# Kernel tuning notes

Hardware: AMD Instinct MI355X
Metric: run time of the kernel (lower is better)

The kernel has to match this reference:

```python
import jax, jax.numpy as jnp
import numpy as np

DIM = 128
B, LQ, LK = 8, 2048, 2048


def setup_inputs() -> dict:
    key = jax.random.key(0)
    k1, k2, k3 = jax.random.split(key, 3)
    output = jax.random.normal(k1, (B, LQ, DIM), dtype=jnp.float32)
    context = jax.random.normal(k2, (B, LK, DIM), dtype=jnp.float32)
    mask = jax.random.randint(k3, (B, LQ, LK), 0, 2).astype(jnp.bool_)
    return {"output": output, "context": context, "mask": mask}


def reference(output, context, mask):
    temperature = jnp.asarray(np.power(DIM, 0.5), dtype=output.dtype)
    # scores: [B, Lq, Lk]
    attn = jnp.einsum('bqd,bkd->bqk', output, context) / temperature
    attn = jnp.where(mask, -jnp.inf, attn)
    out_attn = jax.nn.log_softmax(attn, axis=-1)
    p = jax.nn.softmax(attn, axis=-1)
    # dropout is identity in eval/reference mode
    out = jnp.einsum('bqk,bkd->bqd', p, context)
    return (out, out_attn)
```

## Files before the change

kernel.cpp:

```cpp
#include <hip/hip_runtime.h>
#include <cstdint>


#define DIMV 128
constexpr int BB = 8;
constexpr int LQ = 2048;
constexpr int LK = 2048;
constexpr float RTEMP = 0.08838834764831843f;

typedef _Float16 half8 __attribute__((ext_vector_type(8)));
typedef _Float16 half4v __attribute__((ext_vector_type(4)));
typedef float float4v __attribute__((ext_vector_type(4)));

__global__ void cvt_kernel(const float* __restrict__ q, const float* __restrict__ k,
                           _Float16* __restrict__ q16, _Float16* __restrict__ k16) {
    int idx = blockIdx.x * blockDim.x + threadIdx.x;
    constexpr int NV = BB * LQ * DIMV / 4;
    const float4* src;
    _Float16* dst;
    int v;
    if (idx < NV) { src = (const float4*)q; dst = q16; v = idx; }
    else          { src = (const float4*)k; dst = k16; v = idx - NV; }
    float4 f = src[v];
    half4v h;
    h[0] = (_Float16)f.x; h[1] = (_Float16)f.y; h[2] = (_Float16)f.z; h[3] = (_Float16)f.w;
    *(half4v*)(dst + (size_t)v * 4) = h;
}

__global__ void transp_kernel(const float* __restrict__ ctx, _Float16* __restrict__ vT) {
    __shared__ _Float16 tile[64][DIMV + 2];
    int b = blockIdx.x >> 5;
    int k0 = (blockIdx.x & 31) * 64;
    const float4* src = (const float4*)(ctx + ((size_t)b * LK + k0) * DIMV);
    for (int i = 0; i < 8; i++) {
        int off = threadIdx.x + i * 256;
        float4 f = src[off];
        int elem = off * 4;
        int row = elem >> 7, col = elem & 127;
        tile[row][col + 0] = (_Float16)f.x;
        tile[row][col + 1] = (_Float16)f.y;
        tile[row][col + 2] = (_Float16)f.z;
        tile[row][col + 3] = (_Float16)f.w;
    }
    __syncthreads();
    int d = threadIdx.x >> 1;
    int koff = (threadIdx.x & 1) * 32;
    _Float16* dst = vT + ((size_t)b * DIMV + d) * LK + k0 + koff;
    for (int c = 0; c < 4; c++) {
        half8 h;
        for (int j = 0; j < 8; j++) h[j] = tile[koff + c * 8 + j][d];
        *(half8*)(dst + c * 8) = h;
    }
}

__global__ __launch_bounds__(256, 1)
void attn_kernel(const unsigned char* __restrict__ mask,
                 const _Float16* __restrict__ q16, const _Float16* __restrict__ k16,
                 const _Float16* __restrict__ vT,
                 float* __restrict__ out, float* __restrict__ out_attn) {
    constexpr int TQ = 32;
    constexpr int SSTR = 2056;
    __shared__ __attribute__((aligned(16))) _Float16 S[TQ * SSTR];
    __shared__ float redm[4][TQ];
    __shared__ float mfin[TQ];

    const int tid  = threadIdx.x;
    const int wave = tid >> 6;
    const int lane = tid & 63;
    const int l16  = lane & 15;
    const int quad = lane >> 4;

    const int b  = blockIdx.x >> 6;
    const int q0 = (blockIdx.x & 63) * TQ;

    const _Float16* qbase = q16 + ((size_t)b * LQ + q0) * DIMV;
    const _Float16* kbase = k16 + (size_t)b * LK * DIMV;

    half8 afrag[2][4];
    for (int rt = 0; rt < 2; rt++)
        for (int kk = 0; kk < 4; kk++)
            afrag[rt][kk] = *(const half8*)(qbase + (size_t)(rt * 16 + l16) * DIMV + kk * 32 + quad * 8);

    float mloc[2][4];
    for (int rt = 0; rt < 2; rt++)
        for (int r = 0; r < 4; r++) mloc[rt][r] = -__builtin_inff();

    for (int ch = 0; ch < 8; ch++) {
        const int colbase = wave * 512 + ch * 64;
        float4v acc[4][2];
        for (int ct = 0; ct < 4; ct++)
            for (int rt = 0; rt < 2; rt++)
                acc[ct][rt] = (float4v){0.f, 0.f, 0.f, 0.f};
        for (int ct = 0; ct < 4; ct++) {
            for (int kk = 0; kk < 4; kk++) {
                half8 bf = *(const half8*)(kbase + (size_t)(colbase + ct * 16 + l16) * DIMV + kk * 32 + quad * 8);
                acc[ct][0] = __builtin_amdgcn_mfma_f32_16x16x32_f16(afrag[0][kk], bf, acc[ct][0], 0, 0, 0);
                acc[ct][1] = __builtin_amdgcn_mfma_f32_16x16x32_f16(afrag[1][kk], bf, acc[ct][1], 0, 0, 0);
            }
        }
        for (int ct = 0; ct < 4; ct++)
            for (int rt = 0; rt < 2; rt++)
                for (int r = 0; r < 4; r++) {
                    float v = acc[ct][rt][r] * RTEMP;
                    mloc[rt][r] = fmaxf(mloc[rt][r], v);
                    S[(rt * 16 + quad * 4 + r) * SSTR + colbase + ct * 16 + l16] = (_Float16)v;
                }
    }
    for (int rt = 0; rt < 2; rt++)
        for (int r = 0; r < 4; r++) {
            float v = mloc[rt][r];
            v = fmaxf(v, __shfl_xor(v, 1));
            v = fmaxf(v, __shfl_xor(v, 2));
            v = fmaxf(v, __shfl_xor(v, 4));
            v = fmaxf(v, __shfl_xor(v, 8));
            mloc[rt][r] = v;
        }
    if (l16 == 0)
        for (int rt = 0; rt < 2; rt++)
            for (int r = 0; r < 4; r++)
                redm[wave][rt * 16 + quad * 4 + r] = mloc[rt][r];
    __syncthreads();
    if (tid < TQ) {
        float m = fmaxf(fmaxf(redm[0][tid], redm[1][tid]), fmaxf(redm[2][tid], redm[3][tid]));
        mfin[tid] = m;
    }
    __syncthreads();

    {
        const int row = tid >> 3;
        const int j   = tid & 7;
        const float m = mfin[row];
        const unsigned char* mrow = mask + ((size_t)b * LQ + q0 + row) * LK;
        _Float16* srow = S + row * SSTR;
        const float NEGINF = -__builtin_inff();
        float lsum = 0.f;
        for (int i = 0; i < 32; i++) {
            const int col = i * 64 + j * 8;
            half8 sv = *(half8*)(srow + col);
            unsigned long long mv = *(const unsigned long long*)(mrow + col);
            for (int u = 0; u < 8; u++) {
                float s = (float)sv[u];
                if ((mv >> (8 * u)) & 0xffULL) { s = NEGINF; sv[u] = (_Float16)NEGINF; }
                lsum += __expf(s - m);
            }
            *(half8*)(srow + col) = sv;
        }
        lsum += __shfl_xor(lsum, 1);
        lsum += __shfl_xor(lsum, 2);
        lsum += __shfl_xor(lsum, 4);
        const float logl = __logf(lsum);

        float* oa_row = out_attn + ((size_t)b * LQ + q0 + row) * LK;
        for (int i = 0; i < 32; i++) {
            const int col = i * 64 + j * 8;
            half8 sv = *(half8*)(srow + col);
            half8 pv;
            float lp[8];
            for (int u = 0; u < 8; u++) {
                float s = (float)sv[u];
                float logp = s - m - logl;
                logp = fmaxf(logp, -1.0e30f);
                lp[u] = logp;
                pv[u] = (_Float16)__expf(logp);
            }
            float4 f0 = {lp[0], lp[1], lp[2], lp[3]};
            float4 f1 = {lp[4], lp[5], lp[6], lp[7]};
            *(float4*)(oa_row + col)     = f0;
            *(float4*)(oa_row + col + 4) = f1;
            *(half8*)(srow + col) = pv;
        }
    }
    __syncthreads();

    const _Float16* vbase = vT + (size_t)b * DIMV * LK;
    float4v oacc[2][2];
    for (int ct = 0; ct < 2; ct++)
        for (int rt = 0; rt < 2; rt++)
            oacc[ct][rt] = (float4v){0.f, 0.f, 0.f, 0.f};
    for (int i = 0; i < 64; i++) {
        half8 pa0 = *(half8*)(S + (size_t)(0  + l16) * SSTR + i * 32 + quad * 8);
        half8 pa1 = *(half8*)(S + (size_t)(16 + l16) * SSTR + i * 32 + quad * 8);
        for (int ct = 0; ct < 2; ct++) {
            half8 bf = *(const half8*)(vbase + (size_t)(wave * 32 + ct * 16 + l16) * LK + i * 32 + quad * 8);
            oacc[ct][0] = __builtin_amdgcn_mfma_f32_16x16x32_f16(pa0, bf, oacc[ct][0], 0, 0, 0);
            oacc[ct][1] = __builtin_amdgcn_mfma_f32_16x16x32_f16(pa1, bf, oacc[ct][1], 0, 0, 0);
        }
    }
    for (int ct = 0; ct < 2; ct++)
        for (int rt = 0; rt < 2; rt++)
            for (int r = 0; r < 4; r++)
                out[((size_t)b * LQ + q0 + rt * 16 + quad * 4 + r) * DIMV + wave * 32 + ct * 16 + l16] = oacc[ct][rt][r];
}

extern "C" void kernel_launch(void* const* d_in, const int* in_sizes, int n_in,
                              void* d_out, int out_size, void* d_ws, size_t ws_size,
                              hipStream_t stream) {
    const float* q_f32 = (const float*)d_in[0];
    const float* c_f32 = (const float*)d_in[1];
    const unsigned char* mask = (const unsigned char*)d_in[2];

    float* out      = (float*)d_out;
    float* out_attn = out + (size_t)BB * LQ * DIMV;

    _Float16* q16 = (_Float16*)d_ws;
    _Float16* k16 = q16 + (size_t)BB * LQ * DIMV;
    _Float16* vT  = k16 + (size_t)BB * LK * DIMV;

    cvt_kernel<<<4096, 256, 0, stream>>>(q_f32, c_f32, q16, k16);
    transp_kernel<<<BB * (LK / 64), 256, 0, stream>>>(c_f32, vT);
    attn_kernel<<<BB * (LQ / 32), 256, 0, stream>>>(mask, q16, k16, vT, out, out_attn);
}
```

Measured before the change: 330.6 us.

## Halve query tile to 16 rows for two blocks per CU and interleave batches

Shrinks the per-block query tile from 32 to 16 rows, halving the shared-memory score buffer so two blocks can reside per CU, and raises the launch bound accordingly. Block indices now interleave batches so concurrently running blocks spread across batch elements. The softmax pass uses 16 threads per row. In exchange, each K and V fragment loaded from global memory now feeds only one MFMA instead of two, doubling K/V traffic per query row.

```diff
diff --git a/kernel.cpp b/kernel.cpp
--- a/kernel.cpp
+++ b/kernel.cpp
@@ -53,13 +53,13 @@
     }
 }
 
-__global__ __launch_bounds__(256, 1)
+__global__ __launch_bounds__(256, 2)
 void attn_kernel(const unsigned char* __restrict__ mask,
                  const _Float16* __restrict__ q16, const _Float16* __restrict__ k16,
                  const _Float16* __restrict__ vT,
                  float* __restrict__ out, float* __restrict__ out_attn) {
-    constexpr int TQ = 32;
-    constexpr int SSTR = 2056;
+    constexpr int TQ = 16;
+    constexpr int SSTR = 2052;
     __shared__ __attribute__((aligned(16))) _Float16 S[TQ * SSTR];
     __shared__ float redm[4][TQ];
     __shared__ float mfin[TQ];
@@ -70,72 +70,62 @@
     const int l16  = lane & 15;
     const int quad = lane >> 4;
 
-    const int b  = blockIdx.x >> 6;
-    const int q0 = (blockIdx.x & 63) * TQ;
+    const int b  = blockIdx.x & 7;
+    const int q0 = (blockIdx.x >> 3) * TQ;
 
     const _Float16* qbase = q16 + ((size_t)b * LQ + q0) * DIMV;
     const _Float16* kbase = k16 + (size_t)b * LK * DIMV;
 
-    half8 afrag[2][4];
-    for (int rt = 0; rt < 2; rt++)
-        for (int kk = 0; kk < 4; kk++)
-            afrag[rt][kk] = *(const half8*)(qbase + (size_t)(rt * 16 + l16) * DIMV + kk * 32 + quad * 8);
+    half8 afrag[4];
+    for (int kk = 0; kk < 4; kk++)
+        afrag[kk] = *(const half8*)(qbase + (size_t)l16 * DIMV + kk * 32 + quad * 8);
 
-    float mloc[2][4];
-    for (int rt = 0; rt < 2; rt++)
-        for (int r = 0; r < 4; r++) mloc[rt][r] = -__builtin_inff();
+    float mloc[4];
+    for (int r = 0; r < 4; r++) mloc[r] = -__builtin_inff();
 
     for (int ch = 0; ch < 8; ch++) {
         const int colbase = wave * 512 + ch * 64;
-        float4v acc[4][2];
-        for (int ct = 0; ct < 4; ct++)
-            for (int rt = 0; rt < 2; rt++)
-                acc[ct][rt] = (float4v){0.f, 0.f, 0.f, 0.f};
+        float4v acc[4];
+        for (int ct = 0; ct < 4; ct++) acc[ct] = (float4v){0.f, 0.f, 0.f, 0.f};
         for (int ct = 0; ct < 4; ct++) {
             for (int kk = 0; kk < 4; kk++) {
                 half8 bf = *(const half8*)(kbase + (size_t)(colbase + ct * 16 + l16) * DIMV + kk * 32 + quad * 8);
-                acc[ct][0] = __builtin_amdgcn_mfma_f32_16x16x32_f16(afrag[0][kk], bf, acc[ct][0], 0, 0, 0);
-                acc[ct][1] = __builtin_amdgcn_mfma_f32_16x16x32_f16(afrag[1][kk], bf, acc[ct][1], 0, 0, 0);
+                acc[ct] = __builtin_amdgcn_mfma_f32_16x16x32_f16(afrag[kk], bf, acc[ct], 0, 0, 0);
             }
         }
         for (int ct = 0; ct < 4; ct++)
-            for (int rt = 0; rt < 2; rt++)
-                for (int r = 0; r < 4; r++) {
-                    float v = acc[ct][rt][r] * RTEMP;
-                    mloc[rt][r] = fmaxf(mloc[rt][r], v);
-                    S[(rt * 16 + quad * 4 + r) * SSTR + colbase + ct * 16 + l16] = (_Float16)v;
-                }
+            for (int r = 0; r < 4; r++) {
+                float v = acc[ct][r] * RTEMP;
+                mloc[r] = fmaxf(mloc[r], v);
+                S[(quad * 4 + r) * SSTR + colbase + ct * 16 + l16] = (_Float16)v;
+            }
     }
-    for (int rt = 0; rt < 2; rt++)
-        for (int r = 0; r < 4; r++) {
-            float v = mloc[rt][r];
-            v = fmaxf(v, __shfl_xor(v, 1));
-            v = fmaxf(v, __shfl_xor(v, 2));
-            v = fmaxf(v, __shfl_xor(v, 4));
-            v = fmaxf(v, __shfl_xor(v, 8));
-            mloc[rt][r] = v;
-        }
+    for (int r = 0; r < 4; r++) {
+        float v = mloc[r];
+        v = fmaxf(v, __shfl_xor(v, 1));
+        v = fmaxf(v, __shfl_xor(v, 2));
+        v = fmaxf(v, __shfl_xor(v, 4));
+        v = fmaxf(v, __shfl_xor(v, 8));
+        mloc[r] = v;
+    }
     if (l16 == 0)
-        for (int rt = 0; rt < 2; rt++)
-            for (int r = 0; r < 4; r++)
-                redm[wave][rt * 16 + quad * 4 + r] = mloc[rt][r];
+        for (int r = 0; r < 4; r++)
+            redm[wave][quad * 4 + r] = mloc[r];
     __syncthreads();
-    if (tid < TQ) {
-        float m = fmaxf(fmaxf(redm[0][tid], redm[1][tid]), fmaxf(redm[2][tid], redm[3][tid]));
-        mfin[tid] = m;
-    }
+    if (tid < TQ)
+        mfin[tid] = fmaxf(fmaxf(redm[0][tid], redm[1][tid]), fmaxf(redm[2][tid], redm[3][tid]));
     __syncthreads();
 
     {
-        const int row = tid >> 3;
-        const int j   = tid & 7;
+        const int row = tid >> 4;
+        const int j   = tid & 15;
         const float m = mfin[row];
         const unsigned char* mrow = mask + ((size_t)b * LQ + q0 + row) * LK;
         _Float16* srow = S + row * SSTR;
         const float NEGINF = -__builtin_inff();
         float lsum = 0.f;
-        for (int i = 0; i < 32; i++) {
-            const int col = i * 64 + j * 8;
+        for (int i = 0; i < 16; i++) {
+            const int col = i * 128 + j * 8;
             half8 sv = *(half8*)(srow + col);
             unsigned long long mv = *(const unsigned long long*)(mrow + col);
             for (int u = 0; u < 8; u++) {
@@ -148,11 +138,12 @@
         lsum += __shfl_xor(lsum, 1);
         lsum += __shfl_xor(lsum, 2);
         lsum += __shfl_xor(lsum, 4);
+        lsum += __shfl_xor(lsum, 8);
         const float logl = __logf(lsum);
 
         float* oa_row = out_attn + ((size_t)b * LQ + q0 + row) * LK;
-        for (int i = 0; i < 32; i++) {
-            const int col = i * 64 + j * 8;
+        for (int i = 0; i < 16; i++) {
+            const int col = i * 128 + j * 8;
             half8 sv = *(half8*)(srow + col);
             half8 pv;
             float lp[8];
@@ -173,23 +164,18 @@
     __syncthreads();
 
     const _Float16* vbase = vT + (size_t)b * DIMV * LK;
-    float4v oacc[2][2];
-    for (int ct = 0; ct < 2; ct++)
-        for (int rt = 0; rt < 2; rt++)
-            oacc[ct][rt] = (float4v){0.f, 0.f, 0.f, 0.f};
+    float4v oacc[2];
+    for (int ct = 0; ct < 2; ct++) oacc[ct] = (float4v){0.f, 0.f, 0.f, 0.f};
     for (int i = 0; i < 64; i++) {
-        half8 pa0 = *(half8*)(S + (size_t)(0  + l16) * SSTR + i * 32 + quad * 8);
-        half8 pa1 = *(half8*)(S + (size_t)(16 + l16) * SSTR + i * 32 + quad * 8);
+        half8 pa = *(half8*)(S + (size_t)l16 * SSTR + i * 32 + quad * 8);
         for (int ct = 0; ct < 2; ct++) {
             half8 bf = *(const half8*)(vbase + (size_t)(wave * 32 + ct * 16 + l16) * LK + i * 32 + quad * 8);
-            oacc[ct][0] = __builtin_amdgcn_mfma_f32_16x16x32_f16(pa0, bf, oacc[ct][0], 0, 0, 0);
-            oacc[ct][1] = __builtin_amdgcn_mfma_f32_16x16x32_f16(pa1, bf, oacc[ct][1], 0, 0, 0);
+            oacc[ct] = __builtin_amdgcn_mfma_f32_16x16x32_f16(pa, bf, oacc[ct], 0, 0, 0);
         }
     }
     for (int ct = 0; ct < 2; ct++)
-        for (int rt = 0; rt < 2; rt++)
-            for (int r = 0; r < 4; r++)
-                out[((size_t)b * LQ + q0 + rt * 16 + quad * 4 + r) * DIMV + wave * 32 + ct * 16 + l16] = oacc[ct][rt][r];
+        for (int r = 0; r < 4; r++)
+            out[((size_t)b * LQ + q0 + quad * 4 + r) * DIMV + wave * 32 + ct * 16 + l16] = oacc[ct][r];
 }
 
 extern "C" void kernel_launch(void* const* d_in, const int* in_sizes, int n_in,
@@ -208,5 +194,5 @@
 
     cvt_kernel<<<4096, 256, 0, stream>>>(q_f32, c_f32, q16, k16);
     transp_kernel<<<BB * (LK / 64), 256, 0, stream>>>(c_f32, vT);
-    attn_kernel<<<BB * (LQ / 32), 256, 0, stream>>>(mask, q16, k16, vT, out, out_attn);
+    attn_kernel<<<BB * (LQ / 16), 256, 0, stream>>>(mask, q16, k16, vT, out, out_attn);
 }
```

Result: slower. 361.9 us (+9.5%).
